# Optimization experiments

Measured on AMD Instinct MI355X. Metric: run time of the kernel, lower is better.

Reference implementation:

```python
import jax, jax.numpy as jnp
import numpy as np

EPS = 1e-5
H, DA, DM = 8, 64, 128  # num_read_heads, d_address, d_memory

def setup_inputs() -> dict:
    key = jax.random.key(0)
    ks = jax.random.split(key, 10)
    B, T, D, M = 4, 512, 1024, 128
    scale = lambda fan_in: 1.0 / np.sqrt(fan_in)
    return {
        "query": jax.random.normal(ks[0], (B, T, D), jnp.float32),
        "matrix": jax.random.normal(ks[1], (B, M, DA, DM), jnp.float32),
        "normalizer": jax.random.uniform(ks[2], (B, M, DA), jnp.float32),
        "addresses": jax.random.normal(ks[3], (M, DA), jnp.float32),
        "W_access": jax.random.normal(ks[4], (D, H * DA), jnp.float32) * scale(D),
        "b_access": jnp.zeros((H * DA,), jnp.float32),
        "W_read": jax.random.normal(ks[5], (D, H * DA), jnp.float32) * scale(D),
        "b_read": jnp.zeros((H * DA,), jnp.float32),
        "W_merge": jax.random.normal(ks[6], (H * DM, D), jnp.float32) * scale(H * DM),
        "b_merge": jnp.zeros((D,), jnp.float32),
    }

def reference(query, matrix, normalizer, addresses,
              W_access, b_access, W_read, b_read, W_merge, b_merge):
    act = jax.nn.softplus  # linear kernel feature map
    B, T, D = query.shape
    M = matrix.shape[1]

    # head projections -> (B,T,H,DA)
    aq = act((query @ W_access + b_access).reshape(B, T, H, DA))
    rq = act((query @ W_read + b_read).reshape(B, T, H, DA))

    # --- stage 1: linear attention over the num_memories axis ---
    ak = act(addresses)                       # (M,DA) activated keys
    norm_k = jnp.sum(ak, axis=0)              # (DA,) kernel normalizer (shared)
    den1 = jnp.einsum('btha,a->bth', aq, norm_k)[..., None] + EPS  # (B,T,H,1)

    # kernel over flattened matrix values (M, DA*DM)
    kern_m = jnp.einsum('ma,bmx->bax', ak, matrix.reshape(B, M, DA * DM))
    mat2 = jnp.einsum('btha,bax->bthx', aq, kern_m) / den1          # (B,T,H,DA*DM)
    mat2 = mat2.reshape(B, T, H, DA, DM)

    # kernel over normalizer values (M, DA)
    kern_n = jnp.einsum('ma,bmd->bad', ak, normalizer)              # (B,DA,DA)
    norm2 = jnp.einsum('btha,bad->bthd', aq, kern_n) / den1         # (B,T,H,DA)

    # --- stage 2: read from reduced kernel with read query ---
    num = jnp.einsum('btha,bthax->bthx', rq, mat2)                  # (B,T,H,DM)
    den = jnp.einsum('btha,btha->bth', rq, norm2)[..., None] + EPS
    resp = num / den                                                # (B,T,H,DM)

    return resp.reshape(B, T, H * DM) @ W_merge + b_merge           # (B,T,D)
```

## Files before the change

### kernel.cpp

```cpp
#include <hip/hip_runtime.h>
#include <hip/hip_bf16.h>
#include <math.h>

#define EPSF 1e-5f

typedef __attribute__((ext_vector_type(8))) short short8;
typedef __attribute__((ext_vector_type(4))) float f32x4;
typedef _Float16 half8 __attribute__((ext_vector_type(8)));

constexpr int Bc = 4, Tc = 512, Dc = 1024, Mc = 128, Hc = 8, DAc = 64, DMc = 128;
constexpr int BT = Bc * Tc;
constexpr int Xc = DAc * DMc;
constexpr int Rb = Tc * Hc;

__device__ __forceinline__ float softplus_f(float x) {
    return fmaxf(x, 0.f) + log1pf(expf(-fabsf(x)));
}
__device__ __forceinline__ short f2bf(float f) {
    __hip_bfloat16 h = __float2bfloat16(f);
    return *reinterpret_cast<short*>(&h);
}
__device__ __forceinline__ unsigned pk2(float a, float b) {
    return (unsigned)(unsigned short)f2bf(a) | ((unsigned)(unsigned short)f2bf(b) << 16);
}
__device__ __forceinline__ void lds_load16(void* lds, const void* g) {
    __builtin_amdgcn_global_load_lds((const __attribute__((address_space(1))) int*)g,
                                     (__attribute__((address_space(3))) int*)lds, 16, 0, 0);
}

__global__ __launch_bounds__(256) void front_kern(
        const float* __restrict__ addresses,
        const float* __restrict__ matrix,
        const float* __restrict__ normalizer,
        const float* __restrict__ query,
        const float* __restrict__ W_access,
        const float* __restrict__ W_read,
        const float* __restrict__ W_merge,
        _Float16* __restrict__ kern2,
        float* __restrict__ kern_n,
        float* __restrict__ norm_k,
        __hip_bfloat16* __restrict__ qb,
        __hip_bfloat16* __restrict__ WpT,
        __hip_bfloat16* __restrict__ WmT) {
    __shared__ float smem[8192];
    int bid = blockIdx.x;
    int tid = threadIdx.x;

    if (bid < 256) {
        float (*T)[132] = (float(*)[132])smem;
        _Float16 (*At)[40] = (_Float16(*)[40])(smem + 4224);
        int lane = tid & 63, wid = tid >> 6;
        int l15 = lane & 15, lg = lane >> 4;
        int b = bid >> 6, a = bid & 63;
        int wr = wid & 1, wc = wid >> 1;

        half8 bfrag[2][4];
#pragma unroll
        for (int cf = 0; cf < 2; cf++) {
            int a2 = wc * 32 + cf * 16 + l15;
#pragma unroll
            for (int ks = 0; ks < 4; ks++)
#pragma unroll
                for (int j = 0; j < 8; j++) {
                    int mm = ks * 32 + lg * 8 + j;
                    bfrag[cf][ks][j] = (_Float16)softplus_f(addresses[mm * 64 + a2]);
                }
        }

        const float* msrc = matrix + (size_t)b * Mc * Xc + a * DMc;
        int r = tid >> 3, ms = (tid & 7) * 16;
        int tm = tid >> 1, tk0 = (tid & 1) * 16;

        f32x4 acc[4][2];
#pragma unroll
        for (int i = 0; i < 4; i++)
#pragma unroll
            for (int j = 0; j < 2; j++) acc[i][j] = (f32x4){0.f, 0.f, 0.f, 0.f};

        float4 ld[4];
#pragma unroll
        for (int j = 0; j < 4; j++)
            ld[j] = *(const float4*)(msrc + (size_t)r * Xc + ms + j * 4);

        for (int s = 0; s < 4; s++) {
#pragma unroll
            for (int j = 0; j < 4; j++) *(float4*)&T[r][ms + j * 4] = ld[j];
            __syncthreads();
            if (s < 3) {
#pragma unroll
                for (int j = 0; j < 4; j++)
                    ld[j] = *(const float4*)(msrc + (size_t)((s + 1) * 32 + r) * Xc + ms + j * 4);
            }
            {
                half8 lo, hi;
#pragma unroll
                for (int j = 0; j < 8; j++) lo[j] = (_Float16)T[tk0 + j][tm];
#pragma unroll
                for (int j = 0; j < 8; j++) hi[j] = (_Float16)T[tk0 + 8 + j][tm];
                *(half8*)&At[tm][tk0] = lo;
                *(half8*)&At[tm][tk0 + 8] = hi;
            }
            __syncthreads();
#pragma unroll
            for (int rf = 0; rf < 4; rf++) {
                int row = wr * 64 + rf * 16 + l15;
                half8 af = *(const half8*)&At[row][lg * 8];
#pragma unroll
                for (int cf = 0; cf < 2; cf++)
                    acc[rf][cf] = __builtin_amdgcn_mfma_f32_16x16x32_f16(
                        af, bfrag[cf][s], acc[rf][cf], 0, 0, 0);
            }
            __syncthreads();
        }
        _Float16* dst = kern2 + ((size_t)(b * 64 + a)) * Mc * DAc;
#pragma unroll
        for (int rf = 0; rf < 4; rf++)
#pragma unroll
            for (int cf = 0; cf < 2; cf++) {
                int a2 = wc * 32 + cf * 16 + l15;
#pragma unroll
                for (int i = 0; i < 4; i++) {
                    int mrow = wr * 64 + rf * 16 + lg * 4 + i;
                    dst[mrow * DAc + a2] = (_Float16)acc[rf][cf][i];
                }
            }
        return;
    }
    if (bid < 288) {
        int idx = bid - 256;
        int b = idx >> 3, ch = idx & 7;
        for (int i = tid; i < Mc * DAc; i += 256) smem[i] = softplus_f(addresses[i]);
        __syncthreads();
        int d = tid & 63;
        int g = tid >> 6;
        int a2b = ch * 8 + g * 2;
        float acc0 = 0.f, acc1 = 0.f;
        const float* np = normalizer + (size_t)b * Mc * DAc + d;
        for (int mm = 0; mm < Mc; mm++) {
            float v = np[(size_t)mm * DAc];
            acc0 = fmaf(smem[mm * DAc + a2b + 0], v, acc0);
            acc1 = fmaf(smem[mm * DAc + a2b + 1], v, acc1);
        }
        kern_n[((size_t)b * DAc + a2b + 0) * DAc + d] = acc0;
        kern_n[((size_t)b * DAc + a2b + 1) * DAc + d] = acc1;
        return;
    }
    if (bid == 288) {
        for (int i = tid; i < Mc * DAc; i += 256) smem[i] = softplus_f(addresses[i]);
        __syncthreads();
        if (tid < DAc) {
            float s = 0.f;
            for (int mm = 0; mm < Mc; mm++) s += smem[mm * DAc + tid];
            norm_k[tid] = s;
        }
        return;
    }
    if (bid < 2337) {
        int i = ((bid - 289) * 256 + tid) * 4;
        float4 v = *(const float4*)(query + i);
        unsigned* d = (unsigned*)(qb + i);
        d[0] = pk2(v.x, v.y);
        d[1] = pk2(v.z, v.w);
        return;
    }
    float (*tile)[65] = (float(*)[65])smem;
    const float* S; int stride, nb, n0, kt;
    __hip_bfloat16* dst;
    if (bid < 2593) {
        int idx = bid - 2337;
        kt = idx & 15;
        n0 = (idx >> 4) * 64;
        if (n0 < 512) { S = W_access; nb = n0; }
        else          { S = W_read;   nb = n0 - 512; }
        stride = 512;
        dst = WpT;
    } else {
        int idx = bid - 2593;
        kt = idx & 15;
        n0 = (idx >> 4) * 64;
        S = W_merge; nb = n0; stride = 1024;
        dst = WmT;
    }
    {
        int kl = tid >> 2, q = tid & 3;
        const float* src = S + (size_t)(kt * 64 + kl) * stride + nb + q * 16;
#pragma unroll
        for (int j = 0; j < 4; j++) {
            float4 v = *(const float4*)(src + j * 4);
            tile[kl][q * 16 + j * 4 + 0] = v.x;
            tile[kl][q * 16 + j * 4 + 1] = v.y;
            tile[kl][q * 16 + j * 4 + 2] = v.z;
            tile[kl][q * 16 + j * 4 + 3] = v.w;
        }
    }
    __syncthreads();
    {
        int nl = tid >> 2, q = tid & 3;
        unsigned* d = (unsigned*)(dst + (size_t)(n0 + nl) * 1024 + kt * 64 + q * 16);
#pragma unroll
        for (int j = 0; j < 8; j++)
            d[j] = pk2(tile[q * 16 + j * 2][nl], tile[q * 16 + j * 2 + 1][nl]);
    }
}

template <bool SOFTPLUS, typename OutT>
__global__ __launch_bounds__(256) void gemm_bf16(const __hip_bfloat16* __restrict__ A,
                                                 const __hip_bfloat16* __restrict__ BT_,
                                                 const float* __restrict__ bias0,
                                                 const float* __restrict__ bias1, int N0,
                                                 OutT* __restrict__ C, int N, int K) {
    __shared__ short Ab[2][2][64 * 64];
    __shared__ short Bb[2][2][64 * 64];
    int tid = threadIdx.x, lane = tid & 63, wid = tid >> 6;
    int l15 = lane & 15, lg = lane >> 4;
    int rowblk = blockIdx.x * 64, colblk = blockIdx.y * 64;
    int wr = wid & 1, wc = wid >> 1;
    int srow = lane >> 3;
    int sk = ((lane & 7) ^ srow) * 8;

    f32x4 acc[2][2];
#pragma unroll
    for (int i = 0; i < 2; i++)
#pragma unroll
        for (int j = 0; j < 2; j++) acc[i][j] = (f32x4){0.f, 0.f, 0.f, 0.f};

    auto stage = [&](int kbase, int buf, int sub) {
#pragma unroll
        for (int j = 0; j < 2; j++) {
            int c = wid * 2 + j;
            int row = c * 8 + srow;
            lds_load16(&Ab[buf][sub][c * 512], A + (size_t)(rowblk + row) * K + kbase + sk);
            lds_load16(&Bb[buf][sub][c * 512], BT_ + (size_t)(colblk + row) * K + kbase + sk);
        }
    };
    stage(0, 0, 0);
    stage(64, 0, 1);
    __syncthreads();
    int cur = 0;
    int nks = K >> 7;
    for (int ks = 0; ks < nks; ks++) {
        if (ks + 1 < nks) {
            stage((ks + 1) << 7, cur ^ 1, 0);
            stage(((ks + 1) << 7) + 64, cur ^ 1, 1);
        }
#pragma unroll
        for (int sub = 0; sub < 2; sub++) {
#pragma unroll
            for (int kh = 0; kh < 2; kh++) {
                short8 af[2], bfr[2];
#pragma unroll
                for (int rf = 0; rf < 2; rf++) {
                    int row = wr * 32 + rf * 16 + l15;
                    int ksw = (kh * 32 + lg * 8) ^ ((row & 7) << 3);
                    af[rf] = *(const short8*)&Ab[cur][sub][row * 64 + ksw];
                }
#pragma unroll
                for (int cf = 0; cf < 2; cf++) {
                    int col = wc * 32 + cf * 16 + l15;
                    int ksw = (kh * 32 + lg * 8) ^ ((col & 7) << 3);
                    bfr[cf] = *(const short8*)&Bb[cur][sub][col * 64 + ksw];
                }
#pragma unroll
                for (int rf = 0; rf < 2; rf++)
#pragma unroll
                    for (int cf = 0; cf < 2; cf++)
                        acc[rf][cf] = __builtin_amdgcn_mfma_f32_16x16x32_bf16(
                            af[rf], bfr[cf], acc[rf][cf], 0, 0, 0);
            }
        }
        __syncthreads();
        cur ^= 1;
    }
#pragma unroll
    for (int cf = 0; cf < 2; cf++) {
        int col = colblk + wc * 32 + cf * 16 + l15;
        float bv = (col < N0) ? bias0[col] : bias1[col - N0];
#pragma unroll
        for (int rf = 0; rf < 2; rf++) {
            int rbase = rowblk + wr * 32 + rf * 16 + lg * 4;
#pragma unroll
            for (int i = 0; i < 4; i++) {
                float v = acc[rf][cf][i] + bv;
                if (SOFTPLUS) v = softplus_f(v);
                C[(size_t)(rbase + i) * N + col] = (OutT)v;
            }
        }
    }
}

__global__ __launch_bounds__(256) void k4_mfma(const _Float16* __restrict__ aqrq16,
                                               const _Float16* __restrict__ kern2,
                                               const float* __restrict__ kern_n,
                                               const float* __restrict__ norm_k,
                                               __hip_bfloat16* __restrict__ resp) {
    __shared__ _Float16 Bb[2][2][64 * 64];
    __shared__ _Float16 rql[64][72];
    __shared__ float scl[64];
    __shared__ float nkl[64];
    int tid = threadIdx.x, lane = tid & 63, wid = tid >> 6;
    int l15 = lane & 15, lg = lane >> 4;
    int b = blockIdx.x >> 7;
    int rc = (blockIdx.x >> 1) & 63;
    int mh = blockIdx.x & 1;
    int rowbase = rc * 64;
    int wr = wid & 1, wc = wid >> 1;
    float* knl = (float*)&Bb[1][0][0];

    auto stageB = [&](int a_, int buf, int sl) {
#pragma unroll
        for (int j = 0; j < 2; j++) {
            int c = wid * 2 + j;
            int m = c * 8 + (lane >> 3);
            int sa = ((lane & 7) ^ (lane >> 3)) * 8;
            lds_load16(&Bb[buf][sl][c * 512],
                       kern2 + (((size_t)(b * 64 + a_)) * Mc + mh * 64 + m) * DAc + sa);
        }
    };
    stageB(0, 0, 0);
    stageB(1, 0, 1);
    {
#pragma unroll
        for (int j = 0; j < 4; j++) {
            int c = wid * 4 + j;
            lds_load16(knl + c * 256, kern_n + (size_t)b * 4096 + c * 256 + lane * 4);
        }
    }

    half8 aqp[2][2];
#pragma unroll
    for (int rf = 0; rf < 2; rf++)
#pragma unroll
        for (int kh = 0; kh < 2; kh++) {
            int rg = rowbase + wr * 32 + rf * 16 + l15;
            int t_ = rg >> 3, h = rg & 7;
            aqp[rf][kh] = *(const half8*)(aqrq16 + ((size_t)(b * Tc + t_)) * 1024
                                          + h * 64 + kh * 32 + lg * 8);
        }
    {
        int row = tid >> 2, q = tid & 3;
        int rg = rowbase + row;
        int t_ = rg >> 3, h = rg & 7;
        const _Float16* src = aqrq16 + ((size_t)(b * Tc + t_)) * 1024 + 512 + h * 64 + q * 16;
        *(half8*)&rql[row][q * 16] = *(const half8*)(src);
        *(half8*)&rql[row][q * 16 + 8] = *(const half8*)(src + 8);
    }
    if (tid < 64) nkl[tid] = norm_k[tid];
    __syncthreads();

    {
        int row = wid * 16 + (lane >> 2);
        int c = lane & 3;
        int rg = rowbase + row;
        int t_ = rg >> 3, h = rg & 7;
        const _Float16* aqg = aqrq16 + ((size_t)(b * Tc + t_)) * 1024 + h * 64;
        float accj[16];
#pragma unroll
        for (int j = 0; j < 16; j++) accj[j] = 0.f;
        float d1 = 0.f;
#pragma unroll
        for (int a2c = 0; a2c < 4; a2c++) {
            half8 aa0 = *(const half8*)(aqg + a2c * 16);
            half8 aa1 = *(const half8*)(aqg + a2c * 16 + 8);
            float aqv[16];
#pragma unroll
            for (int j = 0; j < 8; j++) { aqv[j] = (float)aa0[j]; aqv[8 + j] = (float)aa1[j]; }
#pragma unroll
            for (int a2l = 0; a2l < 16; a2l++) {
                int a2 = a2c * 16 + a2l;
                float av = aqv[a2l];
                d1 = fmaf(av, nkl[a2], d1);
                const float4* kr = (const float4*)(knl + a2 * 64 + c * 16);
#pragma unroll
                for (int j4 = 0; j4 < 4; j4++) {
                    float4 kv = kr[j4];
                    accj[j4 * 4 + 0] = fmaf(av, kv.x, accj[j4 * 4 + 0]);
                    accj[j4 * 4 + 1] = fmaf(av, kv.y, accj[j4 * 4 + 1]);
                    accj[j4 * 4 + 2] = fmaf(av, kv.z, accj[j4 * 4 + 2]);
                    accj[j4 * 4 + 3] = fmaf(av, kv.w, accj[j4 * 4 + 3]);
                }
            }
        }
        float sn = 0.f;
#pragma unroll
        for (int j = 0; j < 16; j++)
            sn = fmaf((float)rql[row][c * 16 + j], accj[j], sn);
        sn += __shfl_xor(sn, 1);
        sn += __shfl_xor(sn, 2);
        if (c == 0) {
            float den1 = d1 + EPSF;
            float den = sn / den1 + EPSF;
            scl[row] = 1.f / (den1 * den);
        }
    }
    __syncthreads();

    f32x4 acc[2][2];
#pragma unroll
    for (int i = 0; i < 2; i++)
#pragma unroll
        for (int j = 0; j < 2; j++) acc[i][j] = (f32x4){0.f, 0.f, 0.f, 0.f};

    int cur = 0;
    for (int it = 0; it < 32; it++) {
        if (it < 31) {
            stageB(it * 2 + 2, cur ^ 1, 0);
            stageB(it * 2 + 3, cur ^ 1, 1);
        }
#pragma unroll
        for (int as = 0; as < 2; as++) {
            int a = it * 2 + as;
            _Float16 h0 = rql[wr * 32 + l15][a];
            _Float16 h1 = rql[wr * 32 + 16 + l15][a];
            half8 rb0 = {h0, h0, h0, h0, h0, h0, h0, h0};
            half8 rb1 = {h1, h1, h1, h1, h1, h1, h1, h1};
#pragma unroll
            for (int kh = 0; kh < 2; kh++) {
#pragma unroll
                for (int cf = 0; cf < 2; cf++) {
                    int mloc = wc * 32 + cf * 16 + l15;
                    int ch = (kh * 4 + lg) ^ (mloc & 7);
                    half8 bf = *(const half8*)&Bb[cur][as][mloc * 64 + ch * 8];
                    acc[0][cf] = __builtin_amdgcn_mfma_f32_16x16x32_f16(
                        aqp[0][kh] * rb0, bf, acc[0][cf], 0, 0, 0);
                    acc[1][cf] = __builtin_amdgcn_mfma_f32_16x16x32_f16(
                        aqp[1][kh] * rb1, bf, acc[1][cf], 0, 0, 0);
                }
            }
        }
        __syncthreads();
        cur ^= 1;
    }
#pragma unroll
    for (int rf = 0; rf < 2; rf++) {
#pragma unroll
        for (int i = 0; i < 4; i++) {
            int rl = wr * 32 + rf * 16 + lg * 4 + i;
            int rg = rowbase + rl;
            float s = scl[rl];
            int t_ = rg >> 3, h = rg & 7;
            __hip_bfloat16* dst = resp + ((size_t)(b * Tc + t_)) * 1024 + h * DMc + mh * 64;
#pragma unroll
            for (int cf = 0; cf < 2; cf++) {
                int m = wc * 32 + cf * 16 + l15;
                dst[m] = __float2bfloat16(acc[rf][cf][i] * s);
            }
        }
    }
}

extern "C" void kernel_launch(void* const* d_in, const int* in_sizes, int n_in,
                              void* d_out, int out_size, void* d_ws, size_t ws_size,
                              hipStream_t stream) {
    const float* query      = (const float*)d_in[0];
    const float* matrix     = (const float*)d_in[1];
    const float* normalizer = (const float*)d_in[2];
    const float* addresses  = (const float*)d_in[3];
    const float* W_access   = (const float*)d_in[4];
    const float* b_access   = (const float*)d_in[5];
    const float* W_read     = (const float*)d_in[6];
    const float* b_read     = (const float*)d_in[7];
    const float* W_merge    = (const float*)d_in[8];
    const float* b_merge    = (const float*)d_in[9];
    float* out = (float*)d_out;
    (void)in_sizes; (void)n_in; (void)out_size; (void)ws_size;

    float* ws     = (float*)d_ws;
    float* norm_k = ws;
    float* kern_n = ws + 128;
    _Float16* aqrq16 = (_Float16*)(ws + 16512);
    _Float16* kern2  = (_Float16*)(ws + 1065088);
    __hip_bfloat16* qb   = (__hip_bfloat16*)(ws + 2113664);
    __hip_bfloat16* resp = (__hip_bfloat16*)(ws + 3162240);
    __hip_bfloat16* WpT  = (__hip_bfloat16*)(ws + 4210816);
    __hip_bfloat16* WmT  = (__hip_bfloat16*)(ws + 4735104);

    hipLaunchKernelGGL(front_kern, dim3(2849), dim3(256), 0, stream,
                       addresses, matrix, normalizer, query,
                       W_access, W_read, W_merge,
                       kern2, kern_n, norm_k, qb, WpT, WmT);
    hipLaunchKernelGGL((gemm_bf16<true, _Float16>), dim3(32, 16), dim3(256), 0, stream,
                       qb, WpT, b_access, b_read, 512, aqrq16, 1024, 1024);
    hipLaunchKernelGGL(k4_mfma, dim3(512), dim3(256), 0, stream,
                       aqrq16, kern2, kern_n, norm_k, resp);
    hipLaunchKernelGGL((gemm_bf16<false, float>), dim3(32, 16), dim3(256), 0, stream,
                       resp, WmT, b_merge, b_merge, 2048, out, 1024, 1024);
}
```

Before: 93.53 us.

## Load kern2 B-fragments directly into registers with 4-deep prefetch instead of LDS

The stage-2 MFMA kernel no longer stages kern2 tiles through double-buffered shared memory. Each lane now loads its B fragments straight from global memory into a 4-slot register ring that is refilled four address steps ahead. This removes the per-iteration __syncthreads and the LDS round trip, and it also hoists the A-operand scaling out of the inner column loop. In exchange it uses many more vector registers, which may lower occupancy, and the global loads are no longer shared across waves, so kern2 is fetched redundantly and relies on cache.

```diff
diff --git a/kernel.cpp b/kernel.cpp
--- a/kernel.cpp
+++ b/kernel.cpp
@@ -293,8 +293,8 @@
                                                const float* __restrict__ kern_n,
                                                const float* __restrict__ norm_k,
                                                __hip_bfloat16* __restrict__ resp) {
-    __shared__ _Float16 Bb[2][2][64 * 64];
     __shared__ _Float16 rql[64][72];
+    __shared__ float knl[4096];
     __shared__ float scl[64];
     __shared__ float nkl[64];
     int tid = threadIdx.x, lane = tid & 63, wid = tid >> 6;
@@ -304,20 +304,20 @@
     int mh = blockIdx.x & 1;
     int rowbase = rc * 64;
     int wr = wid & 1, wc = wid >> 1;
-    float* knl = (float*)&Bb[1][0][0];
-
-    auto stageB = [&](int a_, int buf, int sl) {
-#pragma unroll
-        for (int j = 0; j < 2; j++) {
-            int c = wid * 2 + j;
-            int m = c * 8 + (lane >> 3);
-            int sa = ((lane & 7) ^ (lane >> 3)) * 8;
-            lds_load16(&Bb[buf][sl][c * 512],
-                       kern2 + (((size_t)(b * 64 + a_)) * Mc + mh * 64 + m) * DAc + sa);
-        }
+
+    const _Float16* k2base = kern2 + ((size_t)b * 64 * Mc + mh * 64) * DAc
+                             + (wc * 32 + l15) * DAc + lg * 8;
+    half8 Bf[4][2][2];
+    auto loadB = [&](int a_, int slot) {
+        const _Float16* p = k2base + (size_t)a_ * Mc * DAc;
+#pragma unroll
+        for (int kh = 0; kh < 2; kh++)
+#pragma unroll
+            for (int cf = 0; cf < 2; cf++)
+                Bf[slot][kh][cf] = *(const half8*)(p + cf * 16 * DAc + kh * 32);
     };
-    stageB(0, 0, 0);
-    stageB(1, 0, 1);
+    loadB(0, 0); loadB(1, 1); loadB(2, 2); loadB(3, 3);
+
     {
 #pragma unroll
         for (int j = 0; j < 4; j++) {
@@ -325,7 +325,6 @@
             lds_load16(knl + c * 256, kern_n + (size_t)b * 4096 + c * 256 + lane * 4);
         }
     }
-
     half8 aqp[2][2];
 #pragma unroll
     for (int rf = 0; rf < 2; rf++)
@@ -400,35 +399,28 @@
 #pragma unroll
         for (int j = 0; j < 2; j++) acc[i][j] = (f32x4){0.f, 0.f, 0.f, 0.f};
 
-    int cur = 0;
-    for (int it = 0; it < 32; it++) {
-        if (it < 31) {
-            stageB(it * 2 + 2, cur ^ 1, 0);
-            stageB(it * 2 + 3, cur ^ 1, 1);
-        }
-#pragma unroll
-        for (int as = 0; as < 2; as++) {
-            int a = it * 2 + as;
+    for (int it = 0; it < 16; it++) {
+#pragma unroll
+        for (int s = 0; s < 4; s++) {
+            int a = it * 4 + s;
             _Float16 h0 = rql[wr * 32 + l15][a];
             _Float16 h1 = rql[wr * 32 + 16 + l15][a];
             half8 rb0 = {h0, h0, h0, h0, h0, h0, h0, h0};
             half8 rb1 = {h1, h1, h1, h1, h1, h1, h1, h1};
 #pragma unroll
             for (int kh = 0; kh < 2; kh++) {
+                half8 a0 = aqp[0][kh] * rb0;
+                half8 a1 = aqp[1][kh] * rb1;
 #pragma unroll
                 for (int cf = 0; cf < 2; cf++) {
-                    int mloc = wc * 32 + cf * 16 + l15;
-                    int ch = (kh * 4 + lg) ^ (mloc & 7);
-                    half8 bf = *(const half8*)&Bb[cur][as][mloc * 64 + ch * 8];
                     acc[0][cf] = __builtin_amdgcn_mfma_f32_16x16x32_f16(
-                        aqp[0][kh] * rb0, bf, acc[0][cf], 0, 0, 0);
+                        a0, Bf[s][kh][cf], acc[0][cf], 0, 0, 0);
                     acc[1][cf] = __builtin_amdgcn_mfma_f32_16x16x32_f16(
-                        aqp[1][kh] * rb1, bf, acc[1][cf], 0, 0, 0);
-                }
-            }
-        }
-        __syncthreads();
-        cur ^= 1;
+                        a1, Bf[s][kh][cf], acc[1][cf], 0, 0, 0);
+                }
+            }
+            if (it < 15) loadB(a + 4, s);
+        }
     }
 #pragma unroll
     for (int rf = 0; rf < 2; rf++) {
```

After: 123.9 us. +32.5%, slower.
